# Performance work log

Hardware: AMD Instinct MI355X
Metric: run time of the kernel (lower is better)

Reference implementation:

```python
import jax, jax.numpy as jnp
import numpy as np

# DRAW-SN dims (enc_size must equal dec_size: mu/sigma Linears declared on dec_size are applied to h_enc)
T, A, B, N = 16, 128, 128, 32
Z, DEC, ENC = 512, 2048, 2048
BATCH = 512
IN_ENC = 2 * N * N + DEC
LOG2PI = float(np.log(2.0 * np.pi))


def setup_inputs() -> dict:
    key = jax.random.key(0)
    k = jax.random.split(key, 14)
    s = 0.02
    return {
        "x": jax.random.uniform(k[0], (BATCH, A * B), dtype=jnp.float32),
        "eps": jax.random.normal(k[1], (T, BATCH, Z), dtype=jnp.float32),
        # PyTorch LSTMCell weights, gate order (i,f,g,o); b = b_ih + b_hh merged
        "enc_Wih": jax.random.normal(k[2], (4 * ENC, IN_ENC), dtype=jnp.float32) * s,
        "enc_Whh": jax.random.normal(k[3], (4 * ENC, ENC), dtype=jnp.float32) * s,
        "enc_b": jax.random.normal(k[4], (4 * ENC,), dtype=jnp.float32) * s,
        "dec_Wih": jax.random.normal(k[5], (4 * DEC, Z), dtype=jnp.float32) * s,
        "dec_Whh": jax.random.normal(k[6], (4 * DEC, DEC), dtype=jnp.float32) * s,
        "dec_b": jax.random.normal(k[7], (4 * DEC,), dtype=jnp.float32) * s,
        "mu_W": jax.random.normal(k[8], (Z, ENC), dtype=jnp.float32) * s,
        "mu_b": jnp.zeros((Z,), jnp.float32),
        "sig_W": jax.random.normal(k[9], (Z, ENC), dtype=jnp.float32) * s,
        "sig_b": jnp.zeros((Z,), jnp.float32),
        "attn_W": jax.random.normal(k[10], (5, DEC), dtype=jnp.float32) * s,
        "attn_b": jnp.zeros((5,), jnp.float32),
        "w_W": jax.random.normal(k[11], (N * N, DEC), dtype=jnp.float32) * s,
        "w_b": jnp.zeros((N * N,), jnp.float32),
    }


def _lstm(xin, h, c, Wih, Whh, b):
    g = xin @ Wih.T + h @ Whh.T + b
    i, f, gg, o = jnp.split(g, 4, axis=1)
    c_new = jax.nn.sigmoid(f) * c + jax.nn.sigmoid(i) * jnp.tanh(gg)
    h_new = jax.nn.sigmoid(o) * jnp.tanh(c_new)
    return h_new, c_new


def _attn(h_dec, attn_W, attn_b):
    p = h_dec @ attn_W.T + attn_b  # (batch, 5)
    gx = (A + 1) / 2 * (p[:, 0] + 1)
    gy = (B + 1) / 2 * (p[:, 1] + 1)
    sigma2 = jnp.exp(p[:, 2])
    delta = (max(A, B) - 1) / (N - 1) * jnp.exp(p[:, 3])
    gamma = jnp.exp(p[:, 4])
    rng = jnp.arange(N, dtype=p.dtype) - N / 2 - 0.5
    mu_x = gx[:, None] + rng * delta[:, None]  # (batch, N)
    mu_y = gy[:, None] + rng * delta[:, None]

    def fmat(size, mu):
        grid = jnp.arange(size, dtype=p.dtype)
        t = (grid[None, None, :] - mu[:, :, None]) / (2 * sigma2[:, None, None])
        F = jnp.exp(-t * t)  # (batch, N, size)
        return F / (jnp.sum(F, axis=2, keepdims=True) + 1e-9)

    return fmat(A, mu_x), fmat(B, mu_y), gamma


def _glimpse(img, Fx, Fy, bsz):
    # Fy (b,N,B) @ img (b,B,A) @ Fx^T (b,A,N) -> (b,N,N)
    return jnp.einsum('bnB,bBa,bma->bnm', Fy, img.reshape(bsz, B, A), Fx).reshape(bsz, N * N)


def _mdl(h):
    # getHistoryStats (history=None -> stats of h itself, COMP=0) + getMDL with RN=True, s=ones
    mean = jnp.mean(h)
    std = jnp.std(h, ddof=1)
    log_p = -0.5 * ((h - mean) / std) ** 2 - jnp.log(std) - 0.5 * LOG2PI
    lse = jax.nn.logsumexp(log_p)
    # both branches of the COMP update equal log(exp(COMP) + sum exp(log_p)) with COMP=0
    COMP = jnp.logaddexp(jnp.float32(0.0), lse)
    l = COMP - lse  # log(s)=0 for s=ones
    return l * h


def reference(x, eps, enc_Wih, enc_Whh, enc_b, dec_Wih, dec_Whh, dec_b,
              mu_W, mu_b, sig_W, sig_b, attn_W, attn_b, w_W, w_b):
    bsz = x.shape[0]

    def step(carry, e):
        h_enc, c_enc, h_dec, c_dec, canvas = carry
        x_hat = x - jax.nn.sigmoid(canvas)
        # read
        Fx, Fy, gamma = _attn(h_dec, attn_W, attn_b)
        r = jnp.concatenate([_glimpse(x, Fx, Fy, bsz) * gamma[:, None],
                             _glimpse(x_hat, Fx, Fy, bsz) * gamma[:, None]], axis=1)
        # encoder + MDL renorm
        h_enc, c_enc = _lstm(jnp.concatenate([r, h_dec], axis=1), h_enc, c_enc,
                             enc_Wih, enc_Whh, enc_b)
        h_enc = _mdl(h_enc)
        # sampleQ
        mu = h_enc @ mu_W.T + mu_b
        sigma = jnp.exp(h_enc @ sig_W.T + sig_b)
        z = mu + sigma * e
        # decoder + MDL renorm
        h_dec_new, c_dec = _lstm(z, h_dec, c_dec, dec_Wih, dec_Whh, dec_b)
        h_dec_new = _mdl(h_dec_new)
        # write: Fy^T @ w @ Fx -> (b,B,A), divided by gamma
        Fx2, Fy2, gamma2 = _attn(h_dec_new, attn_W, attn_b)
        w = (h_dec_new @ w_W.T + w_b).reshape(bsz, N, N)
        wr = jnp.einsum('bnB,bnm,bma->bBa', Fy2, w, Fx2).reshape(bsz, A * B)
        canvas = canvas + wr / gamma2[:, None]
        return (h_enc, c_enc, h_dec_new, c_dec, canvas), None

    init = (jnp.zeros((bsz, ENC), x.dtype), jnp.zeros((bsz, ENC), x.dtype),
            jnp.zeros((bsz, DEC), x.dtype), jnp.zeros((bsz, DEC), x.dtype),
            jnp.zeros((bsz, A * B), x.dtype))
    carry, _ = jax.lax.scan(step, init, eps)
    return carry[4]  # final canvas cs[T-1], shape (batch, A*B)
```

## Files before the change

kernel.cpp:

```cpp
#include <hip/hip_runtime.h>
#include <math.h>

#define BSZ   512
#define TSTEPS 16
#define HID   2048
#define G4    8192
#define ZD    512
#define ABF   16384
#define ENCK  6144
#define DECK  2560
#define LOG2PI_F 1.8378770664093453f

typedef float  f32x4  __attribute__((ext_vector_type(4)));
typedef __bf16 bf16x8 __attribute__((ext_vector_type(8)));
typedef unsigned short u16;
typedef u16 u16x4 __attribute__((ext_vector_type(4)));
typedef u16 u16x8v __attribute__((ext_vector_type(8)));
union bfcast { u16x8v u; bf16x8 b; };

__device__ __forceinline__ u16 f2bf(float f){
  union { float f; unsigned u; } v; v.f = f;
  unsigned u = v.u;
  return (u16)((u + 0x7FFFu + ((u >> 16) & 1u)) >> 16);
}
__device__ __forceinline__ float bf2f(u16 u){
  union { unsigned u; float f; } v; v.u = ((unsigned)u) << 16; return v.f;
}
__device__ __forceinline__ float sigm(float x){ return 1.f/(1.f + expf(-x)); }

__device__ __forceinline__ void load_lds16(const void* g, void* l){
  __builtin_amdgcn_global_load_lds(
      (const __attribute__((address_space(1))) void*)g,
      (__attribute__((address_space(3))) void*)l, 16, 0, 0);
}

__device__ __forceinline__ float wsum(float v){
  #pragma unroll
  for (int o = 32; o; o >>= 1) v += __shfl_down(v, o, 64);
  return v;
}

__global__ __launch_bounds__(256) void zero_kernel(float* __restrict__ p, int n4){
  int i = blockIdx.x*256 + threadIdx.x;
  const int st = gridDim.x*256;
  f32x4 z = {0.f,0.f,0.f,0.f};
  for (; i < n4; i += st) ((f32x4*)p)[i] = z;
}

__global__ __launch_bounds__(256) void cvt_kernel(const float* __restrict__ s, u16* __restrict__ d, int n4){
  int i = blockIdx.x*256 + threadIdx.x;
  const int st = gridDim.x*256;
  for (; i < n4; i += st){
    f32x4 v = ((const f32x4*)s)[i];
    u16x4 o;
    o[0]=f2bf(v[0]); o[1]=f2bf(v[1]); o[2]=f2bf(v[2]); o[3]=f2bf(v[3]);
    ((u16x4*)d)[i] = o;
  }
}

__global__ __launch_bounds__(256) void cvt_strided_kernel(
    const float* __restrict__ s, u16* __restrict__ d,
    int n4, int sh, int cmask, int dstride, int coloff)
{
  int i = blockIdx.x*256 + threadIdx.x;
  const int st = gridDim.x*256;
  for (; i < n4; i += st){
    f32x4 v = ((const f32x4*)s)[i];
    u16x4 o;
    o[0]=f2bf(v[0]); o[1]=f2bf(v[1]); o[2]=f2bf(v[2]); o[3]=f2bf(v[3]);
    const int row = i >> sh;
    const int c4  = i & cmask;
    *(u16x4*)&d[(size_t)row*dstride + coloff + c4*4] = o;
  }
}

__global__ __launch_bounds__(256) void read_fused(
    const u16* __restrict__ x_bf, const float* __restrict__ canvas,
    const u16* __restrict__ hd, const float* __restrict__ attnW,
    const float* __restrict__ attn_b, u16* __restrict__ r_out)
{
  const int b = blockIdx.x;
  const int tid = threadIdx.x;
  const int wave = tid >> 6;
  const int lane = tid & 63;
  const int lr = lane & 15;
  const int lq = lane >> 4;
  __shared__ float red[4][5];
  __shared__ float prm[5];
  __shared__ float rowsum[32][9];
  __shared__ __align__(16) u16 Fxb[32*128];
  __shared__ __align__(16) u16 Fyb[32*128];
  __shared__ __align__(16) u16 Ttx[32*136];
  __shared__ __align__(16) u16 Ttxh[32*136];

  {
    float a0=0,a1=0,a2=0,a3=0,a4=0;
    const u16* h = hd + (size_t)b*DECK;
    for (int k = tid; k < HID; k += 256){
      const float hv = bf2f(h[k]);
      a0 += hv*attnW[k];
      a1 += hv*attnW[HID + k];
      a2 += hv*attnW[2*HID + k];
      a3 += hv*attnW[3*HID + k];
      a4 += hv*attnW[4*HID + k];
    }
    a0 = wsum(a0); a1 = wsum(a1); a2 = wsum(a2); a3 = wsum(a3); a4 = wsum(a4);
    if (lane == 0){
      red[wave][0]=a0; red[wave][1]=a1; red[wave][2]=a2; red[wave][3]=a3; red[wave][4]=a4;
    }
  }
  __syncthreads();
  if (tid < 5){
    const float p = red[0][tid]+red[1][tid]+red[2][tid]+red[3][tid] + attn_b[tid];
    float v;
    if (tid <= 1)      v = 64.5f*(p + 1.f);
    else if (tid == 2) v = 1.f/(2.f*expf(p));
    else if (tid == 3) v = (127.f/31.f)*expf(p);
    else               v = expf(p);
    prm[tid] = v;
  }
  __syncthreads();
  const float gx = prm[0], gy = prm[1], i2s = prm[2], dl = prm[3], gm = prm[4];

  auto genF = [&](float g0, u16* dst){
    const int rr = tid >> 3;
    const int asub = tid & 7;
    const float mu = g0 + ((float)rr - 16.5f)*dl;
    float s = 0.f;
    for (int a = asub*16; a < asub*16 + 16; a++){
      const float t = ((float)a - mu)*i2s;
      s += expf(-t*t);
    }
    rowsum[rr][asub] = s;
    __syncthreads();
    if (tid < 32){
      float tot = 0.f;
      #pragma unroll
      for (int j = 0; j < 8; j++) tot += rowsum[tid][j];
      rowsum[tid][8] = 1.f/(tot + 1e-9f);
    }
    __syncthreads();
    for (int i = tid; i < 4096; i += 256){
      const int n = i >> 7, a = i & 127;
      const float mu2 = g0 + ((float)n - 16.5f)*dl;
      const float t = ((float)a - mu2)*i2s;
      const float v = expf(-t*t)*rowsum[n][8];
      const int pos = (a >> 3) ^ (n & 7);
      dst[n*128 + pos*8 + (a & 7)] = f2bf(v);
    }
    __syncthreads();
  };
  genF(gx, Fxb);
  genF(gy, Fyb);

  const u16*   xb = x_bf   + (size_t)b*ABF;
  const float* cb = canvas + (size_t)b*ABF;
  f32x4 Cx[2][2], Ch[2][2];
  #pragma unroll
  for (int i = 0; i < 2; i++)
    #pragma unroll
    for (int j = 0; j < 2; j++){ Cx[i][j] = (f32x4){0,0,0,0}; Ch[i][j] = (f32x4){0,0,0,0}; }

  #pragma unroll
  for (int mt = 0; mt < 2; mt++){
    const int row = wave*32 + mt*16 + lr;
    bfcast ax[4], ah[4];
    #pragma unroll
    for (int ks = 0; ks < 4; ks++){
      const int base = row*128 + ks*32 + lq*8;
      ax[ks].u = *(const u16x8v*)&xb[base];
      f32x4 c0 = *(const f32x4*)&cb[base];
      f32x4 c1 = *(const f32x4*)&cb[base + 4];
      #pragma unroll
      for (int j = 0; j < 4; j++){
        ah[ks].u[j]   = f2bf(bf2f(ax[ks].u[j])   - sigm(c0[j]));
        ah[ks].u[4+j] = f2bf(bf2f(ax[ks].u[4+j]) - sigm(c1[j]));
      }
    }
    #pragma unroll
    for (int nt = 0; nt < 2; nt++){
      #pragma unroll
      for (int ks = 0; ks < 4; ks++){
        const int pos = (ks*4 + lq) ^ (lr & 7);
        bf16x8 bf_ = *(const bf16x8*)&Fxb[(nt*16 + lr)*128 + pos*8];
        Cx[mt][nt] = __builtin_amdgcn_mfma_f32_16x16x32_bf16(ax[ks].b, bf_, Cx[mt][nt], 0, 0, 0);
        Ch[mt][nt] = __builtin_amdgcn_mfma_f32_16x16x32_bf16(ah[ks].b, bf_, Ch[mt][nt], 0, 0, 0);
      }
    }
  }
  #pragma unroll
  for (int mt = 0; mt < 2; mt++)
    #pragma unroll
    for (int nt = 0; nt < 2; nt++)
      #pragma unroll
      for (int r = 0; r < 4; r++){
        const int m  = nt*16 + lr;
        const int B_ = wave*32 + mt*16 + lq*4 + r;
        Ttx[m*136 + B_]  = f2bf(Cx[mt][nt][r]);
        Ttxh[m*136 + B_] = f2bf(Ch[mt][nt][r]);
      }
  __syncthreads();

  const int mat = wave >> 1;
  const u16* Tt = mat ? Ttxh : Ttx;
  const int ntl = wave & 1;
  f32x4 R[2];
  R[0] = (f32x4){0,0,0,0}; R[1] = (f32x4){0,0,0,0};
  #pragma unroll
  for (int ks = 0; ks < 4; ks++){
    const int pos = (ks*4 + lq) ^ (lr & 7);
    bf16x8 af = *(const bf16x8*)&Fyb[(ntl*16 + lr)*128 + pos*8];
    #pragma unroll
    for (int mt = 0; mt < 2; mt++){
      bf16x8 bf_ = *(const bf16x8*)&Tt[(mt*16 + lr)*136 + ks*32 + lq*8];
      R[mt] = __builtin_amdgcn_mfma_f32_16x16x32_bf16(af, bf_, R[mt], 0, 0, 0);
    }
  }
  #pragma unroll
  for (int mt = 0; mt < 2; mt++){
    const int m = mt*16 + lr;
    #pragma unroll
    for (int r = 0; r < 4; r++){
      const int n = ntl*16 + lq*4 + r;
      r_out[(size_t)b*ENCK + mat*1024 + n*32 + m] = f2bf(R[mt][r]*gm);
    }
  }
}

struct Slice { const u16* A; const u16* W; const u16* Whi; float* C; int lda, ldw, K, pad; };
struct Slices { Slice s[4]; };

template<int BM, int BN>
__global__ __launch_bounds__(256) void gemm_bt(Slices sl, int nsplit, int ldc)
{
  constexpr int BK = 64;
  constexpr int FI = BM/32;
  constexpr int FJ = BN/32;
  __shared__ __align__(16) u16 Asm[BM*BK];
  __shared__ __align__(16) u16 Bsm[BN*BK];
  const int tid  = threadIdx.x;
  const int wave = tid >> 6;
  const int lane = tid & 63;
  const int wm = wave & 1, wn = wave >> 1;
  const int m0 = blockIdx.y * BM;
  const int n0 = blockIdx.x * BN;
  const Slice& sp = sl.s[blockIdx.z];
  const u16* Ap = sp.A;
  const u16* Wp = sp.W;
  const int lda = sp.lda, ldw = sp.ldw, K = sp.K;
  if (nsplit > 0 && n0 >= nsplit) Wp = sp.Whi - (size_t)nsplit * ldw;
  float* C = sp.C;

  f32x4 acc[FI][FJ];
  #pragma unroll
  for (int i = 0; i < FI; i++)
    #pragma unroll
    for (int j = 0; j < FJ; j++) acc[i][j] = (f32x4){0.f,0.f,0.f,0.f};

  const int lr = lane & 15;
  const int lq = lane >> 4;

  for (int kt = 0; kt < K; kt += BK){
    __syncthreads();
    constexpr int NCA = BM*BK/8;
    #pragma unroll
    for (int it = 0; it < NCA/256; it++){
      const int cb = it*256 + wave*64;
      const int c  = cb + lane;
      const int row = c >> 3;
      const int c8  = (c & 7) ^ (row & 7);
      load_lds16(Ap + (size_t)(m0 + row)*lda + kt + c8*8, &Asm[cb*8]);
    }
    constexpr int NCB = BN*BK/8;
    #pragma unroll
    for (int it = 0; it < NCB/256; it++){
      const int cb = it*256 + wave*64;
      const int c  = cb + lane;
      const int row = c >> 3;
      const int c8  = (c & 7) ^ (row & 7);
      load_lds16(Wp + (size_t)(n0 + row)*ldw + kt + c8*8, &Bsm[cb*8]);
    }
    __syncthreads();
    #pragma unroll
    for (int ks = 0; ks < 2; ks++){
      bf16x8 af[FI], bfr[FJ];
      #pragma unroll
      for (int i = 0; i < FI; i++){
        const int row = wm*(BM/2) + i*16 + lr;
        const int xx = (ks*4 + lq) ^ (row & 7);
        af[i] = *(const bf16x8*)&Asm[row*BK + xx*8];
      }
      #pragma unroll
      for (int j = 0; j < FJ; j++){
        const int row = wn*(BN/2) + j*16 + lr;
        const int xx = (ks*4 + lq) ^ (row & 7);
        bfr[j] = *(const bf16x8*)&Bsm[row*BK + xx*8];
      }
      #pragma unroll
      for (int i = 0; i < FI; i++)
        #pragma unroll
        for (int j = 0; j < FJ; j++)
          acc[i][j] = __builtin_amdgcn_mfma_f32_16x16x32_bf16(af[i], bfr[j], acc[i][j], 0, 0, 0);
    }
  }
  #pragma unroll
  for (int i = 0; i < FI; i++){
    const int gm = m0 + wm*(BM/2) + i*16 + lq*4;
    #pragma unroll
    for (int j = 0; j < FJ; j++){
      const int gn = n0 + wn*(BN/2) + j*16 + lr;
      #pragma unroll
      for (int r = 0; r < 4; r++)
        C[(size_t)(gm + r)*ldc + gn] = acc[i][j][r];
    }
  }
}

__global__ __launch_bounds__(512, 2) void gemm256(Slices sl, int ldc)
{
  __shared__ __align__(16) u16 Asm[2][256*64];
  __shared__ __align__(16) u16 Bsm[2][256*64];
  const int tid  = threadIdx.x;
  const int wave = tid >> 6;
  const int lane = tid & 63;
  const int lr = lane & 15;
  const int lq = lane >> 4;
  const int wm = wave >> 2;
  const int wn = wave & 3;

  const int bid = blockIdx.x;
  const int wg  = (bid & 7)*32 + (bid >> 3);
  const int bx  = wg & 31;
  const int by  = (wg >> 5) & 1;
  const int bz  = wg >> 6;
  const int m0 = by*256, n0 = bx*256;
  const Slice& sp = sl.s[bz];
  const u16* __restrict__ Ap = sp.A;
  const u16* __restrict__ Wp = sp.W;
  float* __restrict__ C = sp.C;
  const int lda = sp.lda, ldw = sp.ldw;
  const int nt = sp.K >> 6;

  f32x4 acc[8][4];
  #pragma unroll
  for (int i = 0; i < 8; i++)
    #pragma unroll
    for (int j = 0; j < 4; j++) acc[i][j] = (f32x4){0.f,0.f,0.f,0.f};

  auto stage = [&](int kt, int bsel){
    const int kcol = kt << 6;
    #pragma unroll
    for (int it = 0; it < 4; it++){
      const int cbk = it*512 + wave*64;
      const int c   = cbk + lane;
      const int row = c >> 3;
      const int c8  = (c & 7) ^ (row & 7);
      load_lds16(Ap + (size_t)(m0 + row)*lda + kcol + c8*8, &Asm[bsel][cbk*8]);
    }
    #pragma unroll
    for (int it = 0; it < 4; it++){
      const int cbk = it*512 + wave*64;
      const int c   = cbk + lane;
      const int row = c >> 3;
      const int c8  = (c & 7) ^ (row & 7);
      load_lds16(Wp + (size_t)(n0 + row)*ldw + kcol + c8*8, &Bsm[bsel][cbk*8]);
    }
  };

  stage(0, 0);
  for (int t = 0; t < nt; t++){
    const int cur = t & 1;
    if (t + 1 < nt){
      stage(t + 1, cur ^ 1);
      __builtin_amdgcn_sched_barrier(0);
      asm volatile("s_waitcnt vmcnt(8)" ::: "memory");
    } else {
      asm volatile("s_waitcnt vmcnt(0)" ::: "memory");
    }
    __builtin_amdgcn_s_barrier();
    __builtin_amdgcn_sched_barrier(0);

    bf16x8 bfr[2][4];
    #pragma unroll
    for (int ks = 0; ks < 2; ks++)
      #pragma unroll
      for (int j = 0; j < 4; j++){
        const int row = wn*64 + j*16 + lr;
        const int xx = (ks*4 + lq) ^ (row & 7);
        bfr[ks][j] = *(const bf16x8*)&Bsm[cur][row*64 + xx*8];
      }
    #pragma unroll
    for (int i = 0; i < 8; i++){
      const int row = wm*128 + i*16 + lr;
      const bf16x8 a0 = *(const bf16x8*)&Asm[cur][row*64 + ((lq    ) ^ (row & 7))*8];
      const bf16x8 a1 = *(const bf16x8*)&Asm[cur][row*64 + ((4 + lq) ^ (row & 7))*8];
      __builtin_amdgcn_s_setprio(1);
      #pragma unroll
      for (int j = 0; j < 4; j++){
        acc[i][j] = __builtin_amdgcn_mfma_f32_16x16x32_bf16(a0, bfr[0][j], acc[i][j], 0, 0, 0);
        acc[i][j] = __builtin_amdgcn_mfma_f32_16x16x32_bf16(a1, bfr[1][j], acc[i][j], 0, 0, 0);
      }
      __builtin_amdgcn_s_setprio(0);
    }
    __builtin_amdgcn_sched_barrier(0);
    __builtin_amdgcn_s_barrier();
  }

  #pragma unroll
  for (int i = 0; i < 8; i++){
    const int gmr = m0 + wm*128 + i*16 + lq*4;
    #pragma unroll
    for (int j = 0; j < 4; j++){
      const int gn = n0 + wn*64 + j*16 + lr;
      #pragma unroll
      for (int r = 0; r < 4; r++)
        C[(size_t)(gmr + r)*ldc + gn] = acc[i][j][r];
    }
  }
}

__global__ __launch_bounds__(256) void lstm_kernel(
    const float* __restrict__ g, const float* __restrict__ bias,
    float* __restrict__ c, float* __restrict__ h, float* __restrict__ ps)
{
  const int idx = blockIdx.x*256 + threadIdx.x;
  const int m = idx >> 9;
  const int q = idx & 511;
  const size_t gb = (size_t)m*G4 + q*4;
  const float* g1 = g + 4194304;
  const float* g2 = g + 2*4194304;
  const float* g3 = g + 3*4194304;
  f32x4 gi = *(const f32x4*)&g[gb]         + *(const f32x4*)&g1[gb]         + *(const f32x4*)&g2[gb]         + *(const f32x4*)&g3[gb]         + *(const f32x4*)&bias[q*4];
  f32x4 gf = *(const f32x4*)&g[gb+HID]     + *(const f32x4*)&g1[gb+HID]     + *(const f32x4*)&g2[gb+HID]     + *(const f32x4*)&g3[gb+HID]     + *(const f32x4*)&bias[HID+q*4];
  f32x4 gg = *(const f32x4*)&g[gb+2*HID]   + *(const f32x4*)&g1[gb+2*HID]   + *(const f32x4*)&g2[gb+2*HID]   + *(const f32x4*)&g3[gb+2*HID]   + *(const f32x4*)&bias[2*HID+q*4];
  f32x4 go = *(const f32x4*)&g[gb+3*HID]   + *(const f32x4*)&g1[gb+3*HID]   + *(const f32x4*)&g2[gb+3*HID]   + *(const f32x4*)&g3[gb+3*HID]   + *(const f32x4*)&bias[3*HID+q*4];
  const size_t cb = (size_t)m*HID + q*4;
  f32x4 cv = *(const f32x4*)&c[cb];
  f32x4 cn, hn;
  #pragma unroll
  for (int k = 0; k < 4; k++){
    const float ck = sigm(gf[k])*cv[k] + sigm(gi[k])*tanhf(gg[k]);
    cn[k] = ck;
    hn[k] = sigm(go[k])*tanhf(ck);
  }
  *(f32x4*)&c[cb] = cn;
  *(f32x4*)&h[cb] = hn;
  float s1 = hn[0]+hn[1]+hn[2]+hn[3];
  float s2 = hn[0]*hn[0]+hn[1]*hn[1]+hn[2]*hn[2]+hn[3]*hn[3];
  s1 = wsum(s1); s2 = wsum(s2);
  __shared__ float r1[4], r2[4];
  const int w = threadIdx.x >> 6;
  if ((threadIdx.x & 63) == 0){ r1[w] = s1; r2[w] = s2; }
  __syncthreads();
  if (threadIdx.x == 0){
    ps[blockIdx.x]        = r1[0]+r1[1]+r1[2]+r1[3];
    ps[1024 + blockIdx.x] = r2[0]+r2[1]+r2[2]+r2[3];
  }
}

__global__ __launch_bounds__(256) void sumexp_kernel(
    const float* __restrict__ h, const float* __restrict__ ps, float* __restrict__ pe)
{
  const int tid = threadIdx.x;
  float t1 = 0.f, t2 = 0.f;
  for (int i = tid; i < 1024; i += 256){ t1 += ps[i]; t2 += ps[1024 + i]; }
  t1 = wsum(t1); t2 = wsum(t2);
  __shared__ float r1[4], r2[4];
  const int w = tid >> 6;
  if ((tid & 63) == 0){ r1[w] = t1; r2[w] = t2; }
  __syncthreads();
  __shared__ float mh[2];
  if (tid == 0){
    const float S1 = r1[0]+r1[1]+r1[2]+r1[3];
    const float S2 = r2[0]+r2[1]+r2[2]+r2[3];
    const float mean = S1*(1.f/1048576.f);
    const float var  = (S2 - 1048576.f*mean*mean)*(1.f/1048575.f);
    mh[0] = mean; mh[1] = 1.f/sqrtf(var);
  }
  __syncthreads();
  const float mean = mh[0], istd = mh[1];
  float se = 0.f;
  for (int i = blockIdx.x*256 + tid; i < (1<<18); i += 256*256){
    f32x4 v = ((const f32x4*)h)[i];
    #pragma unroll
    for (int k = 0; k < 4; k++){
      const float u = (v[k] - mean)*istd;
      se += expf(-0.5f*u*u);
    }
  }
  se = wsum(se);
  __shared__ float r3[4];
  if ((tid & 63) == 0) r3[w] = se;
  __syncthreads();
  if (tid == 0) pe[blockIdx.x] = r3[0]+r3[1]+r3[2]+r3[3];
}

__global__ __launch_bounds__(256) void scale_kernel(
    const float* __restrict__ h, const float* __restrict__ ps,
    const float* __restrict__ pe, u16* __restrict__ d1, int ld1,
    u16* __restrict__ d2, int ld2)
{
  const int tid = threadIdx.x;
  float t1 = 0.f, t2 = 0.f;
  for (int i = tid; i < 1024; i += 256){ t1 += ps[i]; t2 += ps[1024 + i]; }
  float t3 = pe[tid];
  t1 = wsum(t1); t2 = wsum(t2); t3 = wsum(t3);
  __shared__ float r1[4], r2[4], r3[4];
  const int w = tid >> 6;
  if ((tid & 63) == 0){ r1[w] = t1; r2[w] = t2; r3[w] = t3; }
  __syncthreads();
  __shared__ float lsh;
  if (tid == 0){
    const float S1 = r1[0]+r1[1]+r1[2]+r1[3];
    const float S2 = r2[0]+r2[1]+r2[2]+r2[3];
    const float SE = r3[0]+r3[1]+r3[2]+r3[3];
    const float mean = S1*(1.f/1048576.f);
    const float var  = (S2 - 1048576.f*mean*mean)*(1.f/1048575.f);
    const float stdv = sqrtf(var);
    const float lse = logf(SE) - logf(stdv) - 0.5f*LOG2PI_F;
    lsh = fmaxf(-lse, 0.f) + log1pf(expf(-fabsf(lse)));
  }
  __syncthreads();
  const float l = lsh;
  const int i = blockIdx.x*256 + tid;
  const int row = i >> 9;
  const int c4  = i & 511;
  f32x4 v = ((const f32x4*)h)[i];
  u16x4 o;
  #pragma unroll
  for (int k = 0; k < 4; k++) o[k] = f2bf(v[k]*l);
  *(u16x4*)&d1[(size_t)row*ld1 + c4*4] = o;
  if (d2) *(u16x4*)&d2[(size_t)row*ld2 + c4*4] = o;
}

__global__ __launch_bounds__(256) void z_kernel(
    const float* __restrict__ zp, const float* __restrict__ mu_b,
    const float* __restrict__ sig_b, const float* __restrict__ ep, u16* __restrict__ zo)
{
  const int idx = blockIdx.x*256 + threadIdx.x;
  const int m = idx >> 7;
  const int q = idx & 127;
  const size_t base = (size_t)m*1024 + q*4;
  f32x4 mu = *(const f32x4*)&zp[base] + *(const f32x4*)&zp[524288 + base]
           + *(const f32x4*)&zp[2*524288 + base] + *(const f32x4*)&zp[3*524288 + base]
           + *(const f32x4*)&mu_b[q*4];
  f32x4 ls = *(const f32x4*)&zp[base+512] + *(const f32x4*)&zp[524288 + base+512]
           + *(const f32x4*)&zp[2*524288 + base+512] + *(const f32x4*)&zp[3*524288 + base+512]
           + *(const f32x4*)&sig_b[q*4];
  f32x4 ev = *(const f32x4*)&ep[(size_t)m*512 + q*4];
  u16x4 o;
  #pragma unroll
  for (int k = 0; k < 4; k++) o[k] = f2bf(mu[k] + expf(ls[k])*ev[k]);
  *(u16x4*)&zo[(size_t)m*DECK + q*4] = o;
}

__global__ __launch_bounds__(256) void write_fused(
    const float* __restrict__ wp, const float* __restrict__ w_b,
    const u16* __restrict__ hd, const float* __restrict__ attnW,
    const float* __restrict__ attn_b, float* __restrict__ canvas)
{
  const int b = blockIdx.x;
  const int tid = threadIdx.x;
  __shared__ float red[4][5];
  __shared__ float prm[5];
  __shared__ float inv[32];
  __shared__ float sW[1024];
  __shared__ __align__(16) float sF[32*132];
  __shared__ float sU[128*33];

  {
    float a0=0,a1=0,a2=0,a3=0,a4=0;
    const u16* h = hd + (size_t)b*DECK;
    for (int k = tid; k < HID; k += 256){
      const float hv = bf2f(h[k]);
      a0 += hv*attnW[k];
      a1 += hv*attnW[HID + k];
      a2 += hv*attnW[2*HID + k];
      a3 += hv*attnW[3*HID + k];
      a4 += hv*attnW[4*HID + k];
    }
    a0 = wsum(a0); a1 = wsum(a1); a2 = wsum(a2); a3 = wsum(a3); a4 = wsum(a4);
    if ((tid & 63) == 0){
      const int w = tid >> 6;
      red[w][0]=a0; red[w][1]=a1; red[w][2]=a2; red[w][3]=a3; red[w][4]=a4;
    }
  }
  for (int i = tid; i < 1024; i += 256)
    sW[i] = wp[(size_t)b*1024 + i] + wp[524288 + (size_t)b*1024 + i]
          + wp[2*524288 + (size_t)b*1024 + i] + wp[3*524288 + (size_t)b*1024 + i] + w_b[i];
  __syncthreads();
  if (tid < 5){
    const float p = red[0][tid]+red[1][tid]+red[2][tid]+red[3][tid] + attn_b[tid];
    float v;
    if (tid <= 1)      v = 64.5f*(p + 1.f);
    else if (tid == 2) v = 1.f/(2.f*expf(p));
    else if (tid == 3) v = (127.f/31.f)*expf(p);
    else               v = expf(p);
    prm[tid] = v;
  }
  __syncthreads();
  const float gx = prm[0], gy = prm[1], i2s = prm[2], dl = prm[3], gm = prm[4];

  auto genF = [&](float g0){
    for (int i = tid; i < 4096; i += 256){
      const int n = i >> 7, a = i & 127;
      const float mu = g0 + ((float)n - 16.5f)*dl;
      const float t = ((float)a - mu)*i2s;
      sF[n*132 + a] = expf(-t*t);
    }
    __syncthreads();
    if (tid < 32){
      float ssum = 0.f;
      for (int a = 0; a < 128; a++) ssum += sF[tid*132 + a];
      inv[tid] = 1.f/(ssum + 1e-9f);
    }
    __syncthreads();
    for (int i = tid; i < 4096; i += 256)
      sF[(i >> 7)*132 + (i & 127)] *= inv[i >> 7];
    __syncthreads();
  };

  genF(gy);
  {
    const int Bg = tid & 31, mg = tid >> 5;
    float acc[4][4] = {};
    for (int n = 0; n < 32; n++){
      float fy[4], wv[4];
      #pragma unroll
      for (int i = 0; i < 4; i++) fy[i] = sF[n*132 + Bg + 32*i];
      #pragma unroll
      for (int j = 0; j < 4; j++) wv[j] = sW[n*32 + mg*4 + j];
      #pragma unroll
      for (int i = 0; i < 4; i++)
        #pragma unroll
        for (int j = 0; j < 4; j++) acc[i][j] += fy[i]*wv[j];
    }
    #pragma unroll
    for (int i = 0; i < 4; i++)
      #pragma unroll
      for (int j = 0; j < 4; j++)
        sU[(Bg + 32*i)*33 + mg*4 + j] = acc[i][j];
  }
  __syncthreads();
  genF(gx);
  {
    const int Bg = tid & 31, ag = tid >> 5;
    float acc[64];
    #pragma unroll
    for (int k = 0; k < 64; k++) acc[k] = 0.f;
    for (int mm = 0; mm < 32; mm++){
      float u[4];
      #pragma unroll
      for (int i = 0; i < 4; i++) u[i] = sU[(Bg + 32*i)*33 + mm];
      f32x4 fx[4];
      #pragma unroll
      for (int k = 0; k < 4; k++) fx[k] = *(const f32x4*)&sF[mm*132 + ag*16 + k*4];
      #pragma unroll
      for (int i = 0; i < 4; i++)
        #pragma unroll
        for (int k = 0; k < 4; k++)
          #pragma unroll
          for (int cc = 0; cc < 4; cc++)
            acc[i*16 + k*4 + cc] += u[i]*fx[k][cc];
    }
    const float ig = 1.f/gm;
    #pragma unroll
    for (int i = 0; i < 4; i++){
      const int B_ = Bg + 32*i;
      #pragma unroll
      for (int k = 0; k < 4; k++){
        float* cp = &canvas[(size_t)b*ABF + B_*128 + ag*16 + k*4];
        f32x4 cv = *(const f32x4*)cp;
        #pragma unroll
        for (int cc = 0; cc < 4; cc++) cv[cc] += acc[i*16 + k*4 + cc]*ig;
        *(f32x4*)cp = cv;
      }
    }
  }
}

extern "C" void kernel_launch(void* const* d_in, const int* in_sizes, int n_in,
                              void* d_out, int out_size, void* d_ws, size_t ws_size,
                              hipStream_t stream)
{
  (void)in_sizes; (void)n_in; (void)out_size; (void)ws_size;
  const float* x      = (const float*)d_in[0];
  const float* eps    = (const float*)d_in[1];
  const float* encWih = (const float*)d_in[2];
  const float* encWhh = (const float*)d_in[3];
  const float* enc_b  = (const float*)d_in[4];
  const float* decWih = (const float*)d_in[5];
  const float* decWhh = (const float*)d_in[6];
  const float* dec_b  = (const float*)d_in[7];
  const float* muW    = (const float*)d_in[8];
  const float* mu_b   = (const float*)d_in[9];
  const float* sigW   = (const float*)d_in[10];
  const float* sig_b  = (const float*)d_in[11];
  const float* attnW  = (const float*)d_in[12];
  const float* attn_b = (const float*)d_in[13];
  const float* wW     = (const float*)d_in[14];
  const float* w_b    = (const float*)d_in[15];
  float* canvas = (float*)d_out;

  char* wsb = (char*)d_ws;
  size_t off = 0;
  auto alloc = [&](size_t bytes)->char*{
    char* p = wsb + off; off += (bytes + 255) & ~(size_t)255; return p;
  };
  float* c_enc = (float*)alloc(1048576*4);
  float* c_dec = (float*)alloc(1048576*4);
  u16*   encA  = (u16*)  alloc((size_t)BSZ*ENCK*2);
  u16*   decA  = (u16*)  alloc((size_t)BSZ*DECK*2);
  const size_t state_bytes = off;
  float* ps    = (float*)alloc(2304*4);
  float* pe    = (float*)alloc(256*4);
  float* h_tmp = (float*)alloc(1048576*4);
  float* g_buf = (float*)alloc((size_t)4*4194304*4);
  float* zbuf  = g_buf;
  float* wbuf  = g_buf + 2097152;
  u16*   x_bf  = (u16*)  alloc((size_t)8388608*2);
  u16* encW    = (u16*)alloc((size_t)G4*ENCK*2);
  u16* decW    = (u16*)alloc((size_t)G4*DECK*2);
  u16* muw_bf  = (u16*)alloc((size_t)1048576*2);
  u16* sigw_bf = (u16*)alloc((size_t)1048576*2);
  u16* ww_bf   = (u16*)alloc((size_t)2097152*2);

  zero_kernel<<<1024, 256, 0, stream>>>((float*)wsb, (int)(state_bytes/16));
  zero_kernel<<<2048, 256, 0, stream>>>(canvas, (ABF/4)*BSZ);
  cvt_kernel<<<2048, 256, 0, stream>>>(x,    x_bf,   8388608/4);
  cvt_strided_kernel<<<2048, 256, 0, stream>>>(encWih, encW, 8388608, 10, 1023, ENCK, 0);
  cvt_strided_kernel<<<2048, 256, 0, stream>>>(encWhh, encW, 4194304,  9,  511, ENCK, 4096);
  cvt_strided_kernel<<<1024, 256, 0, stream>>>(decWih, decW, 1048576,  7,  127, DECK, 0);
  cvt_strided_kernel<<<2048, 256, 0, stream>>>(decWhh, decW, 4194304,  9,  511, DECK, 512);
  cvt_kernel<<<512,  256, 0, stream>>>(muW,  muw_bf,  1048576/4);
  cvt_kernel<<<512,  256, 0, stream>>>(sigW, sigw_bf, 1048576/4);
  cvt_kernel<<<512,  256, 0, stream>>>(wW,   ww_bf,   2097152/4);

  Slices enc_sl = {};
  for (int k = 0; k < 4; k++)
    enc_sl.s[k] = { encA + 1536*k, encW + 1536*k, nullptr, g_buf + (size_t)k*4194304, ENCK, ENCK, 1536, 0 };

  Slices dec_sl = {};
  for (int k = 0; k < 4; k++)
    dec_sl.s[k] = { decA + 640*k, decW + 640*k, nullptr, g_buf + (size_t)k*4194304, DECK, DECK, 640, 0 };

  Slices ms_sl = {}, w_sl = {};
  for (int k = 0; k < 4; k++){
    ms_sl.s[k] = { encA + 4096 + 512*k, muw_bf + 512*k, sigw_bf + 512*k, zbuf + (size_t)k*524288, ENCK, HID, 512, 0 };
    w_sl.s[k]  = { decA + 512  + 512*k, ww_bf  + 512*k, nullptr,         wbuf + (size_t)k*524288, DECK, HID, 512, 0 };
  }

  for (int t = 0; t < TSTEPS; t++){
    read_fused<<<512, 256, 0, stream>>>(x_bf, canvas, decA + 512, attnW, attn_b, encA);
    gemm256<<<256, 512, 0, stream>>>(enc_sl, G4);
    lstm_kernel<<<1024, 256, 0, stream>>>(g_buf, enc_b, c_enc, h_tmp, ps);
    sumexp_kernel<<<256, 256, 0, stream>>>(h_tmp, ps, pe);
    scale_kernel<<<1024, 256, 0, stream>>>(h_tmp, ps, pe, encA + 4096, ENCK, nullptr, 0);
    gemm_bt<64,64><<<dim3(16,8,4), 256, 0, stream>>>(ms_sl, 512, 1024);
    z_kernel<<<256, 256, 0, stream>>>(zbuf, mu_b, sig_b, eps + (size_t)t*BSZ*ZD, decA);
    gemm256<<<256, 512, 0, stream>>>(dec_sl, G4);
    lstm_kernel<<<1024, 256, 0, stream>>>(g_buf, dec_b, c_dec, h_tmp, ps);
    sumexp_kernel<<<256, 256, 0, stream>>>(h_tmp, ps, pe);
    scale_kernel<<<1024, 256, 0, stream>>>(h_tmp, ps, pe, decA + 512, DECK, encA + 2048, ENCK);
    gemm_bt<64,64><<<dim3(16,8,4), 256, 0, stream>>>(w_sl, 0, 1024);
    write_fused<<<512, 256, 0, stream>>>(wbuf, w_b, decA + 512, attnW, attn_b, canvas);
  }
}
```

Measured before the change: 4.137 ms.

## Replace split-K GEMM with 256x128 triple-buffered two-phase pipelined kernel

The big LSTM gate GEMMs now use 256x128 tiles and split K two ways instead of four, with the same 256 blocks. Each block triple-buffers its LDS tiles and splits every K-tile into two half-phases, so loads run two tiles ahead and interleave with MFMA work. Halving the split-K partials cuts the fp32 partial traffic the LSTM kernel has to read. In exchange each block runs a longer K loop with smaller tiles and more barriers per tile.

```diff
diff --git a/kernel.cpp b/kernel.cpp
--- a/kernel.cpp
+++ b/kernel.cpp
@@ -316,24 +316,24 @@
   }
 }
 
-__global__ __launch_bounds__(512, 2) void gemm256(Slices sl, int ldc)
-{
-  __shared__ __align__(16) u16 Asm[2][256*64];
-  __shared__ __align__(16) u16 Bsm[2][256*64];
+__global__ __launch_bounds__(512, 2) void gemm_ph(Slices sl, int ldc)
+{
+  __shared__ __align__(16) u16 Asm[3][256*64];
+  __shared__ __align__(16) u16 Bsm[3][128*64];
   const int tid  = threadIdx.x;
   const int wave = tid >> 6;
   const int lane = tid & 63;
   const int lr = lane & 15;
   const int lq = lane >> 4;
-  const int wm = wave >> 2;
-  const int wn = wave & 3;
+  const int wm = wave >> 1;
+  const int wn = wave & 1;
 
   const int bid = blockIdx.x;
   const int wg  = (bid & 7)*32 + (bid >> 3);
-  const int bx  = wg & 31;
-  const int by  = (wg >> 5) & 1;
-  const int bz  = wg >> 6;
-  const int m0 = by*256, n0 = bx*256;
+  const int bx  = wg & 63;
+  const int by  = (wg >> 6) & 1;
+  const int bz  = wg >> 7;
+  const int m0 = by*256, n0 = bx*128;
   const Slice& sp = sl.s[bz];
   const u16* __restrict__ Ap = sp.A;
   const u16* __restrict__ Wp = sp.W;
@@ -341,24 +341,27 @@
   const int lda = sp.lda, ldw = sp.ldw;
   const int nt = sp.K >> 6;
 
-  f32x4 acc[8][4];
-  #pragma unroll
-  for (int i = 0; i < 8; i++)
+  f32x4 acc[4][4];
+  #pragma unroll
+  for (int i = 0; i < 4; i++)
     #pragma unroll
     for (int j = 0; j < 4; j++) acc[i][j] = (f32x4){0.f,0.f,0.f,0.f};
 
-  auto stage = [&](int kt, int bsel){
+  auto stageA = [&](int kt, int bsel, int half){
     const int kcol = kt << 6;
     #pragma unroll
-    for (int it = 0; it < 4; it++){
-      const int cbk = it*512 + wave*64;
+    for (int it = 0; it < 2; it++){
+      const int cbk = (half*2 + it)*512 + wave*64;
       const int c   = cbk + lane;
       const int row = c >> 3;
       const int c8  = (c & 7) ^ (row & 7);
       load_lds16(Ap + (size_t)(m0 + row)*lda + kcol + c8*8, &Asm[bsel][cbk*8]);
     }
-    #pragma unroll
-    for (int it = 0; it < 4; it++){
+  };
+  auto stageB = [&](int kt, int bsel){
+    const int kcol = kt << 6;
+    #pragma unroll
+    for (int it = 0; it < 2; it++){
       const int cbk = it*512 + wave*64;
       const int c   = cbk + lane;
       const int row = c >> 3;
@@ -367,48 +370,77 @@
     }
   };
 
-  stage(0, 0);
+  stageA(0, 0, 0); stageA(0, 0, 1); stageB(0, 0);
+  stageA(1, 1, 0); stageA(1, 1, 1); stageB(1, 1);
+  asm volatile("s_waitcnt vmcnt(6)" ::: "memory");
+  __builtin_amdgcn_s_barrier();
+
+  int b = 0;
   for (int t = 0; t < nt; t++){
-    const int cur = t & 1;
-    if (t + 1 < nt){
-      stage(t + 1, cur ^ 1);
-      __builtin_amdgcn_sched_barrier(0);
-      asm volatile("s_waitcnt vmcnt(8)" ::: "memory");
-    } else {
-      asm volatile("s_waitcnt vmcnt(0)" ::: "memory");
-    }
-    __builtin_amdgcn_s_barrier();
-    __builtin_amdgcn_sched_barrier(0);
-
-    bf16x8 bfr[2][4];
-    #pragma unroll
-    for (int ks = 0; ks < 2; ks++)
-      #pragma unroll
-      for (int j = 0; j < 4; j++){
-        const int row = wn*64 + j*16 + lr;
-        const int xx = (ks*4 + lq) ^ (row & 7);
-        bfr[ks][j] = *(const bf16x8*)&Bsm[cur][row*64 + xx*8];
-      }
-    #pragma unroll
-    for (int i = 0; i < 8; i++){
-      const int row = wm*128 + i*16 + lr;
-      const bf16x8 a0 = *(const bf16x8*)&Asm[cur][row*64 + ((lq    ) ^ (row & 7))*8];
-      const bf16x8 a1 = *(const bf16x8*)&Asm[cur][row*64 + ((4 + lq) ^ (row & 7))*8];
-      __builtin_amdgcn_s_setprio(1);
-      #pragma unroll
-      for (int j = 0; j < 4; j++){
-        acc[i][j] = __builtin_amdgcn_mfma_f32_16x16x32_bf16(a0, bfr[0][j], acc[i][j], 0, 0, 0);
-        acc[i][j] = __builtin_amdgcn_mfma_f32_16x16x32_bf16(a1, bfr[1][j], acc[i][j], 0, 0, 0);
-      }
-      __builtin_amdgcn_s_setprio(0);
-    }
+    const int bs = (b == 0) ? 2 : b - 1;
+    const bool pf   = (t + 2 < nt);
+    const bool more = (t + 1 < nt);
+
+    bf16x8 a0[4], b0[4];
+    #pragma unroll
+    for (int j = 0; j < 4; j++){
+      const int row = wn*64 + j*16 + lr;
+      b0[j] = *(const bf16x8*)&Bsm[b][row*64 + ((lq) ^ (row & 7))*8];
+    }
+    #pragma unroll
+    for (int i = 0; i < 4; i++){
+      const int row = wm*64 + i*16 + lr;
+      a0[i] = *(const bf16x8*)&Asm[b][row*64 + ((lq) ^ (row & 7))*8];
+    }
+    if (pf){ stageA(t+2, bs, 0); stageA(t+2, bs, 1); }
     __builtin_amdgcn_sched_barrier(0);
     __builtin_amdgcn_s_barrier();
-  }
-
-  #pragma unroll
-  for (int i = 0; i < 8; i++){
-    const int gmr = m0 + wm*128 + i*16 + lq*4;
+    asm volatile("s_waitcnt lgkmcnt(0)" ::: "memory");
+    __builtin_amdgcn_sched_barrier(0);
+    __builtin_amdgcn_s_setprio(1);
+    #pragma unroll
+    for (int i = 0; i < 4; i++)
+      #pragma unroll
+      for (int j = 0; j < 4; j++)
+        acc[i][j] = __builtin_amdgcn_mfma_f32_16x16x32_bf16(a0[i], b0[j], acc[i][j], 0, 0, 0);
+    __builtin_amdgcn_s_setprio(0);
+    __builtin_amdgcn_sched_barrier(0);
+    __builtin_amdgcn_s_barrier();
+
+    bf16x8 a1[4], b1[4];
+    #pragma unroll
+    for (int j = 0; j < 4; j++){
+      const int row = wn*64 + j*16 + lr;
+      b1[j] = *(const bf16x8*)&Bsm[b][row*64 + ((4 + lq) ^ (row & 7))*8];
+    }
+    #pragma unroll
+    for (int i = 0; i < 4; i++){
+      const int row = wm*64 + i*16 + lr;
+      a1[i] = *(const bf16x8*)&Asm[b][row*64 + ((4 + lq) ^ (row & 7))*8];
+    }
+    if (pf) stageB(t+2, bs);
+    __builtin_amdgcn_sched_barrier(0);
+    if (pf)        asm volatile("s_waitcnt vmcnt(6)" ::: "memory");
+    else if (more) asm volatile("s_waitcnt vmcnt(0)" ::: "memory");
+    __builtin_amdgcn_s_barrier();
+    asm volatile("s_waitcnt lgkmcnt(0)" ::: "memory");
+    __builtin_amdgcn_sched_barrier(0);
+    __builtin_amdgcn_s_setprio(1);
+    #pragma unroll
+    for (int i = 0; i < 4; i++)
+      #pragma unroll
+      for (int j = 0; j < 4; j++)
+        acc[i][j] = __builtin_amdgcn_mfma_f32_16x16x32_bf16(a1[i], b1[j], acc[i][j], 0, 0, 0);
+    __builtin_amdgcn_s_setprio(0);
+    __builtin_amdgcn_sched_barrier(0);
+    __builtin_amdgcn_s_barrier();
+
+    b = (b == 2) ? 0 : b + 1;
+  }
+
+  #pragma unroll
+  for (int i = 0; i < 4; i++){
+    const int gmr = m0 + wm*64 + i*16 + lq*4;
     #pragma unroll
     for (int j = 0; j < 4; j++){
       const int gn = n0 + wn*64 + j*16 + lr;
@@ -428,12 +460,10 @@
   const int q = idx & 511;
   const size_t gb = (size_t)m*G4 + q*4;
   const float* g1 = g + 4194304;
-  const float* g2 = g + 2*4194304;
-  const float* g3 = g + 3*4194304;
-  f32x4 gi = *(const f32x4*)&g[gb]         + *(const f32x4*)&g1[gb]         + *(const f32x4*)&g2[gb]         + *(const f32x4*)&g3[gb]         + *(const f32x4*)&bias[q*4];
-  f32x4 gf = *(const f32x4*)&g[gb+HID]     + *(const f32x4*)&g1[gb+HID]     + *(const f32x4*)&g2[gb+HID]     + *(const f32x4*)&g3[gb+HID]     + *(const f32x4*)&bias[HID+q*4];
-  f32x4 gg = *(const f32x4*)&g[gb+2*HID]   + *(const f32x4*)&g1[gb+2*HID]   + *(const f32x4*)&g2[gb+2*HID]   + *(const f32x4*)&g3[gb+2*HID]   + *(const f32x4*)&bias[2*HID+q*4];
-  f32x4 go = *(const f32x4*)&g[gb+3*HID]   + *(const f32x4*)&g1[gb+3*HID]   + *(const f32x4*)&g2[gb+3*HID]   + *(const f32x4*)&g3[gb+3*HID]   + *(const f32x4*)&bias[3*HID+q*4];
+  f32x4 gi = *(const f32x4*)&g[gb]       + *(const f32x4*)&g1[gb]       + *(const f32x4*)&bias[q*4];
+  f32x4 gf = *(const f32x4*)&g[gb+HID]   + *(const f32x4*)&g1[gb+HID]   + *(const f32x4*)&bias[HID+q*4];
+  f32x4 gg = *(const f32x4*)&g[gb+2*HID] + *(const f32x4*)&g1[gb+2*HID] + *(const f32x4*)&bias[2*HID+q*4];
+  f32x4 go = *(const f32x4*)&g[gb+3*HID] + *(const f32x4*)&g1[gb+3*HID] + *(const f32x4*)&bias[3*HID+q*4];
   const size_t cb = (size_t)m*HID + q*4;
   f32x4 cv = *(const f32x4*)&c[cb];
   f32x4 cn, hn;
@@ -715,7 +745,7 @@
   float* ps    = (float*)alloc(2304*4);
   float* pe    = (float*)alloc(256*4);
   float* h_tmp = (float*)alloc(1048576*4);
-  float* g_buf = (float*)alloc((size_t)4*4194304*4);
+  float* g_buf = (float*)alloc((size_t)2*4194304*4);
   float* zbuf  = g_buf;
   float* wbuf  = g_buf + 2097152;
   u16*   x_bf  = (u16*)  alloc((size_t)8388608*2);
@@ -737,12 +767,12 @@
   cvt_kernel<<<512,  256, 0, stream>>>(wW,   ww_bf,   2097152/4);
 
   Slices enc_sl = {};
-  for (int k = 0; k < 4; k++)
-    enc_sl.s[k] = { encA + 1536*k, encW + 1536*k, nullptr, g_buf + (size_t)k*4194304, ENCK, ENCK, 1536, 0 };
+  for (int k = 0; k < 2; k++)
+    enc_sl.s[k] = { encA + 3072*k, encW + 3072*k, nullptr, g_buf + (size_t)k*4194304, ENCK, ENCK, 3072, 0 };
 
   Slices dec_sl = {};
-  for (int k = 0; k < 4; k++)
-    dec_sl.s[k] = { decA + 640*k, decW + 640*k, nullptr, g_buf + (size_t)k*4194304, DECK, DECK, 640, 0 };
+  for (int k = 0; k < 2; k++)
+    dec_sl.s[k] = { decA + 1280*k, decW + 1280*k, nullptr, g_buf + (size_t)k*4194304, DECK, DECK, 1280, 0 };
 
   Slices ms_sl = {}, w_sl = {};
   for (int k = 0; k < 4; k++){
@@ -752,13 +782,13 @@
 
   for (int t = 0; t < TSTEPS; t++){
     read_fused<<<512, 256, 0, stream>>>(x_bf, canvas, decA + 512, attnW, attn_b, encA);
-    gemm256<<<256, 512, 0, stream>>>(enc_sl, G4);
+    gemm_ph<<<256, 512, 0, stream>>>(enc_sl, G4);
     lstm_kernel<<<1024, 256, 0, stream>>>(g_buf, enc_b, c_enc, h_tmp, ps);
     sumexp_kernel<<<256, 256, 0, stream>>>(h_tmp, ps, pe);
     scale_kernel<<<1024, 256, 0, stream>>>(h_tmp, ps, pe, encA + 4096, ENCK, nullptr, 0);
     gemm_bt<64,64><<<dim3(16,8,4), 256, 0, stream>>>(ms_sl, 512, 1024);
     z_kernel<<<256, 256, 0, stream>>>(zbuf, mu_b, sig_b, eps + (size_t)t*BSZ*ZD, decA);
-    gemm256<<<256, 512, 0, stream>>>(dec_sl, G4);
+    gemm_ph<<<256, 512, 0, stream>>>(dec_sl, G4);
     lstm_kernel<<<1024, 256, 0, stream>>>(g_buf, dec_b, c_dec, h_tmp, ps);
     sumexp_kernel<<<256, 256, 0, stream>>>(h_tmp, ps, pe);
     scale_kernel<<<1024, 256, 0, stream>>>(h_tmp, ps, pe, decA + 512, DECK, encA + 2048, ENCK);
```

Result: faster. 3.602 ms (-12.9%).
